# Optimization experiments

Measured on AMD Instinct MI355X. Metric: run time of the kernel, lower is better.

The kernel has to match this reference:

```python
import jax, jax.numpy as jnp
import numpy as np

ALPHA = 0.2  # LeakyReLU negative slope
B, L, FIN, FOUT = 128, 512, 128, 128

def setup_inputs() -> dict:
    key = jax.random.key(0)
    k1, k2, k3, k4, k5 = jax.random.split(key, 5)
    h = jax.random.normal(k1, (B, L, FIN), jnp.float32)
    W = jax.random.normal(k2, (FIN, FOUT), jnp.float32) * (1.0 / np.sqrt(FIN))
    a = jax.random.normal(k3, (2 * FOUT,), jnp.float32) * (1.0 / np.sqrt(2 * FOUT))
    edge_bias = jax.random.normal(k4, (B, L, L), jnp.float32) * 0.1
    adj_mask = jax.random.uniform(k5, (L, L)) > 0.3
    adj_mask = adj_mask | jnp.eye(L, dtype=bool)  # self-loops avoid fully-masked rows
    return {"h": h, "W": W, "a": a, "edge_bias": edge_bias, "adj_mask": adj_mask}

def reference(h, W, a, edge_bias, adj_mask):
    # Wh: [B, L, Fout]
    Wh = jnp.einsum('blf,fo->blo', h, W)
    Fout = W.shape[1]
    # a([Wh_i, Wh_j]) == Wh_i @ a[:Fout] + Wh_j @ a[Fout:]  (avoids O(B*L*L*2F) concat)
    ei = Wh @ a[:Fout]   # [B, L]  (target i contribution)
    ej = Wh @ a[Fout:]   # [B, L]  (source j contribution)
    e = jax.nn.leaky_relu(ei[:, :, None] + ej[:, None, :], ALPHA) + edge_bias  # [B, L, L]
    e = jnp.where(adj_mask[None, :, :], e, -jnp.inf)
    att = jax.nn.softmax(e, axis=-1)  # dropout=0.0 -> identity
    h_prime = jnp.einsum('bij,bjo->bio', att, Wh)  # [B, L, Fout]
    return jax.nn.elu(h_prime)  # concat=True branch
```

## Files before the change

### kernel.cpp

```cpp
#include <hip/hip_runtime.h>
#include <string.h>

#define ALPHA 0.2f

typedef short short8 __attribute__((ext_vector_type(8)));
typedef float floatx4 __attribute__((ext_vector_type(4)));
typedef unsigned short ushort4v __attribute__((ext_vector_type(4)));

__device__ inline unsigned short f2bf(float f) {
    unsigned int v; __builtin_memcpy(&v, &f, 4);
    v = v + 0x7FFFu + ((v >> 16) & 1u);
    return (unsigned short)(v >> 16);
}

#define GLD4(dst, p) asm volatile("global_load_dwordx4 %0, %1, off nt" : "=v"(dst) : "v"(p))

__global__ __launch_bounds__(256, 4) void wh_kernel(const float* __restrict__ h,
                                                    const float* __restrict__ W,
                                                    const float* __restrict__ a,
                                                    const int* __restrict__ adj,
                                                    unsigned short* __restrict__ wht,
                                                    float* __restrict__ ei,
                                                    float* __restrict__ ej,
                                                    unsigned long long* __restrict__ mask)
{
    __shared__ __align__(16) unsigned short w_s[128][136];
    __shared__ float a_s[256];
    const int tid  = threadIdx.x;
    const int lane = tid & 63;
    const int wv   = tid >> 6;
    const int quad = lane >> 4;
    const int l16  = lane & 15;
    const int r0   = blockIdx.x * 128;
    const int b    = r0 >> 9;
    const int jb   = r0 & 511;

    for (int it = 0; it < 64; ++it) {
        int idx = it * 256 + tid;
        w_s[idx & 127][idx >> 7] = f2bf(W[idx]);
    }
    a_s[tid] = a[tid];

    if (blockIdx.x < 128) {
        const int row = blockIdx.x * 4 + wv;
        const int* ar = adj + row * 512;
        unsigned long long wbits[8];
#pragma unroll
        for (int q = 0; q < 8; ++q) wbits[q] = __ballot(ar[q * 64 + lane] != 0);
        if (lane == 0) {
            unsigned long long* mr = mask + row * 8;
#pragma unroll
            for (int q = 0; q < 8; ++q) mr[q] = wbits[q];
        }
    }
    __syncthreads();

    const float* hp0 = h + (size_t)(r0 + wv * 32 + l16) * 128 + quad * 8;
    const float* hp1 = hp0 + 16 * 128;

    floatx4 acc[8][2];
    for (int mo = 0; mo < 8; ++mo)
        for (int n = 0; n < 2; ++n) acc[mo][n] = (floatx4)0.f;

    floatx4 c00 = *(const floatx4*)(hp0);
    floatx4 c01 = *(const floatx4*)(hp0 + 4);
    floatx4 c10 = *(const floatx4*)(hp1);
    floatx4 c11 = *(const floatx4*)(hp1 + 4);
#pragma unroll
    for (int kk = 0; kk < 4; ++kk) {
        floatx4 n00, n01, n10, n11;
        if (kk < 3) {
            n00 = *(const floatx4*)(hp0 + (kk + 1) * 32);
            n01 = *(const floatx4*)(hp0 + (kk + 1) * 32 + 4);
            n10 = *(const floatx4*)(hp1 + (kk + 1) * 32);
            n11 = *(const floatx4*)(hp1 + (kk + 1) * 32 + 4);
        }
        short8 bfr0, bfr1;
#pragma unroll
        for (int e = 0; e < 4; ++e) {
            bfr0[e]     = (short)f2bf(c00[e]);
            bfr0[4 + e] = (short)f2bf(c01[e]);
            bfr1[e]     = (short)f2bf(c10[e]);
            bfr1[4 + e] = (short)f2bf(c11[e]);
        }
#pragma unroll
        for (int mo = 0; mo < 8; ++mo) {
            short8 afr = *(const short8*)&w_s[mo * 16 + l16][kk * 32 + quad * 8];
            acc[mo][0] = __builtin_amdgcn_mfma_f32_16x16x32_bf16(afr, bfr0, acc[mo][0], 0, 0, 0);
            acc[mo][1] = __builtin_amdgcn_mfma_f32_16x16x32_bf16(afr, bfr1, acc[mo][1], 0, 0, 0);
        }
        c00 = n00; c01 = n01; c10 = n10; c11 = n11;
    }

    for (int n = 0; n < 2; ++n) {
        float si = 0.f, sj = 0.f;
        for (int mo = 0; mo < 8; ++mo)
            for (int r = 0; r < 4; ++r) {
                int o = mo * 16 + quad * 4 + r;
                float v = acc[mo][n][r];
                si += v * a_s[o];
                sj += v * a_s[128 + o];
            }
        si += __shfl_xor(si, 16); si += __shfl_xor(si, 32);
        sj += __shfl_xor(sj, 16); sj += __shfl_xor(sj, 32);
        if (quad == 0) {
            int j = jb + wv * 32 + n * 16 + l16;
            ei[b * 512 + j] = si;
            ej[b * 512 + j] = sj;
        }
    }

    for (int mo = 0; mo < 8; ++mo)
        for (int n = 0; n < 2; ++n)
            for (int r = 0; r < 4; ++r) {
                int o = mo * 16 + quad * 4 + r;
                int j = jb + wv * 32 + n * 16 + l16;
                wht[(size_t)b * 65536 + o * 512 + j] = f2bf(acc[mo][n][r]);
            }
}

__global__ __launch_bounds__(512, 4) void attn_kernel(const unsigned short* __restrict__ wht,
                                                      const float* __restrict__ ei,
                                                      const float* __restrict__ ej,
                                                      const float* __restrict__ bias,
                                                      const unsigned* __restrict__ mask32,
                                                      float* __restrict__ out)
{
    __shared__ __align__(16) unsigned short p_s[64][520];
    __shared__ float ei_s[64];
    __shared__ float ej_s[512];
    __shared__ float s_row[64];
    __shared__ unsigned m_s[64][16];

    const int tid  = threadIdx.x;
    const int lane = tid & 63;
    const int wv   = tid >> 6;
    const int quad = lane >> 4;
    const int l16  = lane & 15;

    const int n  = blockIdx.x;
    const int x  = n & 7;
    const int r  = n >> 3;
    const int b  = x * 16 + (r >> 3);
    const int i0 = (r & 7) * 64;

    ej_s[tid] = ej[b * 512 + tid];
    if (tid < 64) ei_s[tid] = ei[b * 512 + i0 + tid];
#pragma unroll
    for (int it = 0; it < 2; ++it) {
        int idx = it * 512 + tid;
        m_s[idx >> 4][idx & 15] = mask32[i0 * 16 + idx];
    }
    __syncthreads();

    const float* bp = bias + ((size_t)(b * 512 + i0 + wv * 8)) * 512;
    const int mw = lane >> 3;
    const int ms = (lane & 7) * 4;

    const floatx4 ejv0 = *(const floatx4*)&ej_s[lane * 4];
    const floatx4 ejv1 = *(const floatx4*)&ej_s[256 + lane * 4];

    floatx4 q0[4], q1[4];
    GLD4(q0[0], bp + lane * 4);            GLD4(q1[0], bp + 256 + lane * 4);
    GLD4(q0[1], bp + 512 + lane * 4);      GLD4(q1[1], bp + 768 + lane * 4);
    GLD4(q0[2], bp + 1024 + lane * 4);     GLD4(q1[2], bp + 1280 + lane * 4);
    GLD4(q0[3], bp + 1536 + lane * 4);     GLD4(q1[3], bp + 1792 + lane * 4);

    float rsum[8];
#pragma unroll
    for (int rr = 0; rr < 8; ++rr) {
        if (rr <= 4)      asm volatile("s_waitcnt vmcnt(6)" ::: "memory");
        else if (rr == 5) asm volatile("s_waitcnt vmcnt(4)" ::: "memory");
        else if (rr == 6) asm volatile("s_waitcnt vmcnt(2)" ::: "memory");
        else              asm volatile("s_waitcnt vmcnt(0)" ::: "memory");
        __builtin_amdgcn_sched_barrier(0);

        const int s  = rr & 3;
        const int il = wv * 8 + rr;
        const float eiv = ei_s[il];
        const unsigned nib0 = (m_s[il][mw]     >> ms) & 0xFu;
        const unsigned nib1 = (m_s[il][8 + mw] >> ms) & 0xFu;
        float sm = 0.f;
        ushort4v p0, p1;
#pragma unroll
        for (int e = 0; e < 4; ++e) {
            float xv = eiv + ejv0[e];
            xv = fmaxf(xv, ALPHA * xv);
            xv += q0[s][e];
            float p = __expf(xv);
            p = (nib0 & (1u << e)) ? p : 0.f;
            sm += p;
            p0[e] = f2bf(p);
        }
#pragma unroll
        for (int e = 0; e < 4; ++e) {
            float xv = eiv + ejv1[e];
            xv = fmaxf(xv, ALPHA * xv);
            xv += q1[s][e];
            float p = __expf(xv);
            p = (nib1 & (1u << e)) ? p : 0.f;
            sm += p;
            p1[e] = f2bf(p);
        }
        *(ushort4v*)&p_s[il][lane * 4]       = p0;
        *(ushort4v*)&p_s[il][256 + lane * 4] = p1;
        rsum[rr] = sm;

        if (rr < 4) {
            GLD4(q0[s], bp + (size_t)(rr + 4) * 512 + lane * 4);
            GLD4(q1[s], bp + (size_t)(rr + 4) * 512 + 256 + lane * 4);
        }
    }

#pragma unroll
    for (int rr = 0; rr < 8; ++rr)
        for (int off = 32; off; off >>= 1)
            rsum[rr] += __shfl_xor(rsum[rr], off);
    if (lane == 0)
#pragma unroll
        for (int rr = 0; rr < 8; ++rr) s_row[wv * 8 + rr] = rsum[rr];
    __syncthreads();

    floatx4 acc[4];
#pragma unroll
    for (int m = 0; m < 4; ++m) acc[m] = (floatx4)0.f;

    const unsigned short* wb = wht + (size_t)b * 65536 + (wv * 16 + l16) * 512 + quad * 8;
    short8 bf = *(const short8*)(wb);
#pragma unroll
    for (int k16 = 0; k16 < 16; ++k16) {
        int ko = k16 * 32 + quad * 8;
        short8 nbf;
        if (k16 < 15) nbf = *(const short8*)(wb + (k16 + 1) * 32);
        short8 af0 = *(const short8*)&p_s[l16][ko];
        short8 af1 = *(const short8*)&p_s[16 + l16][ko];
        short8 af2 = *(const short8*)&p_s[32 + l16][ko];
        short8 af3 = *(const short8*)&p_s[48 + l16][ko];
        acc[0] = __builtin_amdgcn_mfma_f32_16x16x32_bf16(af0, bf, acc[0], 0, 0, 0);
        acc[1] = __builtin_amdgcn_mfma_f32_16x16x32_bf16(af1, bf, acc[1], 0, 0, 0);
        acc[2] = __builtin_amdgcn_mfma_f32_16x16x32_bf16(af2, bf, acc[2], 0, 0, 0);
        acc[3] = __builtin_amdgcn_mfma_f32_16x16x32_bf16(af3, bf, acc[3], 0, 0, 0);
        bf = nbf;
    }

#pragma unroll
    for (int m = 0; m < 4; ++m)
#pragma unroll
        for (int rr2 = 0; rr2 < 4; ++rr2) {
            int il = m * 16 + quad * 4 + rr2;
            int o  = wv * 16 + l16;
            float v = acc[m][rr2] / s_row[il];
            v = v > 0.f ? v : (__expf(v) - 1.f);
            __builtin_nontemporal_store(v, &out[((size_t)(b * 512 + i0 + il)) * 128 + o]);
        }
}

extern "C" void kernel_launch(void* const* d_in, const int* in_sizes, int n_in,
                              void* d_out, int out_size, void* d_ws, size_t ws_size,
                              hipStream_t stream)
{
    const float* h    = (const float*)d_in[0];
    const float* W    = (const float*)d_in[1];
    const float* a    = (const float*)d_in[2];
    const float* bias = (const float*)d_in[3];
    const int*   adj  = (const int*)d_in[4];
    float*       out  = (float*)d_out;

    unsigned short* wht = (unsigned short*)d_ws;
    float* ei = (float*)((char*)d_ws + 16777216);
    float* ej = ei + 65536;
    unsigned long long* mask = (unsigned long long*)((char*)d_ws + 17301504);

    hipLaunchKernelGGL(wh_kernel,   dim3(512),  dim3(256), 0, stream, h, W, a, adj, wht, ei, ej, mask);
    hipLaunchKernelGGL(attn_kernel, dim3(1024), dim3(512), 0, stream, wht, ei, ej, bias,
                       (const unsigned*)mask, out);
}
```

Measured before the change: 241.5 us.

## Warp-specialize attention kernel into producer/consumer waves with double-buffered P tiles

Restructures attn_kernel so each block handles 256 rows of one batch. Four producer waves stream edge_bias and compute masked exp scores into a double-buffered 16-row LDS tile. Four consumer waves run the bf16 MFMA against Wh^T, normalise and apply ELU, and the two groups synchronise with s_barrier per chunk. The aim is to overlap the bandwidth-bound bias streaming with the matmul and to cut the grid to 256 persistent-style blocks. This risks lower occupancy and idle waves if the two phases are unbalanced, and consumers re-read Wh^T from global/L2 on every chunk.

```diff
diff --git a/kernel.cpp b/kernel.cpp
--- a/kernel.cpp
+++ b/kernel.cpp
@@ -119,18 +119,18 @@
             }
 }
 
-__global__ __launch_bounds__(512, 4) void attn_kernel(const unsigned short* __restrict__ wht,
+__global__ __launch_bounds__(512, 2) void attn_kernel(const unsigned short* __restrict__ wht,
                                                       const float* __restrict__ ei,
                                                       const float* __restrict__ ej,
                                                       const float* __restrict__ bias,
                                                       const unsigned* __restrict__ mask32,
                                                       float* __restrict__ out)
 {
-    __shared__ __align__(16) unsigned short p_s[64][520];
-    __shared__ float ei_s[64];
+    __shared__ __align__(16) unsigned short p_s[2][16][520];
+    __shared__ float ei_s[256];
     __shared__ float ej_s[512];
-    __shared__ float s_row[64];
-    __shared__ unsigned m_s[64][16];
+    __shared__ float s_row[2][16];
+    __shared__ unsigned m_s[256][16];
 
     const int tid  = threadIdx.x;
     const int lane = tid & 63;
@@ -138,121 +138,141 @@
     const int quad = lane >> 4;
     const int l16  = lane & 15;
 
-    const int n  = blockIdx.x;
-    const int x  = n & 7;
-    const int r  = n >> 3;
-    const int b  = x * 16 + (r >> 3);
-    const int i0 = (r & 7) * 64;
-
-    ej_s[tid] = ej[b * 512 + tid];
-    if (tid < 64) ei_s[tid] = ei[b * 512 + i0 + tid];
-#pragma unroll
-    for (int it = 0; it < 2; ++it) {
+    const int x     = blockIdx.x & 7;
+    const int r     = blockIdx.x >> 3;
+    const int b     = x * 16 + (r >> 1);
+    const int hrow0 = (r & 1) * 256;
+
+    if (tid < 128) *(floatx4*)&ej_s[tid * 4] = *(const floatx4*)(ej + b * 512 + tid * 4);
+    else if (tid < 384) ei_s[tid - 128] = ei[b * 512 + hrow0 + (tid - 128)];
+#pragma unroll
+    for (int it = 0; it < 8; ++it) {
         int idx = it * 512 + tid;
-        m_s[idx >> 4][idx & 15] = mask32[i0 * 16 + idx];
+        ((unsigned*)m_s)[idx] = mask32[hrow0 * 16 + idx];
     }
     __syncthreads();
 
-    const float* bp = bias + ((size_t)(b * 512 + i0 + wv * 8)) * 512;
     const int mw = lane >> 3;
     const int ms = (lane & 7) * 4;
 
-    const floatx4 ejv0 = *(const floatx4*)&ej_s[lane * 4];
-    const floatx4 ejv1 = *(const floatx4*)&ej_s[256 + lane * 4];
-
-    floatx4 q0[4], q1[4];
-    GLD4(q0[0], bp + lane * 4);            GLD4(q1[0], bp + 256 + lane * 4);
-    GLD4(q0[1], bp + 512 + lane * 4);      GLD4(q1[1], bp + 768 + lane * 4);
-    GLD4(q0[2], bp + 1024 + lane * 4);     GLD4(q1[2], bp + 1280 + lane * 4);
-    GLD4(q0[3], bp + 1536 + lane * 4);     GLD4(q1[3], bp + 1792 + lane * 4);
-
-    float rsum[8];
-#pragma unroll
-    for (int rr = 0; rr < 8; ++rr) {
-        if (rr <= 4)      asm volatile("s_waitcnt vmcnt(6)" ::: "memory");
-        else if (rr == 5) asm volatile("s_waitcnt vmcnt(4)" ::: "memory");
-        else if (rr == 6) asm volatile("s_waitcnt vmcnt(2)" ::: "memory");
-        else              asm volatile("s_waitcnt vmcnt(0)" ::: "memory");
-        __builtin_amdgcn_sched_barrier(0);
-
-        const int s  = rr & 3;
-        const int il = wv * 8 + rr;
-        const float eiv = ei_s[il];
-        const unsigned nib0 = (m_s[il][mw]     >> ms) & 0xFu;
-        const unsigned nib1 = (m_s[il][8 + mw] >> ms) & 0xFu;
-        float sm = 0.f;
-        ushort4v p0, p1;
-#pragma unroll
-        for (int e = 0; e < 4; ++e) {
-            float xv = eiv + ejv0[e];
-            xv = fmaxf(xv, ALPHA * xv);
-            xv += q0[s][e];
-            float p = __expf(xv);
-            p = (nib0 & (1u << e)) ? p : 0.f;
-            sm += p;
-            p0[e] = f2bf(p);
-        }
-#pragma unroll
-        for (int e = 0; e < 4; ++e) {
-            float xv = eiv + ejv1[e];
-            xv = fmaxf(xv, ALPHA * xv);
-            xv += q1[s][e];
-            float p = __expf(xv);
-            p = (nib1 & (1u << e)) ? p : 0.f;
-            sm += p;
-            p1[e] = f2bf(p);
-        }
-        *(ushort4v*)&p_s[il][lane * 4]       = p0;
-        *(ushort4v*)&p_s[il][256 + lane * 4] = p1;
-        rsum[rr] = sm;
-
-        if (rr < 4) {
-            GLD4(q0[s], bp + (size_t)(rr + 4) * 512 + lane * 4);
-            GLD4(q1[s], bp + (size_t)(rr + 4) * 512 + 256 + lane * 4);
-        }
-    }
-
-#pragma unroll
-    for (int rr = 0; rr < 8; ++rr)
-        for (int off = 32; off; off >>= 1)
-            rsum[rr] += __shfl_xor(rsum[rr], off);
-    if (lane == 0)
-#pragma unroll
-        for (int rr = 0; rr < 8; ++rr) s_row[wv * 8 + rr] = rsum[rr];
-    __syncthreads();
-
-    floatx4 acc[4];
-#pragma unroll
-    for (int m = 0; m < 4; ++m) acc[m] = (floatx4)0.f;
-
-    const unsigned short* wb = wht + (size_t)b * 65536 + (wv * 16 + l16) * 512 + quad * 8;
-    short8 bf = *(const short8*)(wb);
-#pragma unroll
-    for (int k16 = 0; k16 < 16; ++k16) {
-        int ko = k16 * 32 + quad * 8;
-        short8 nbf;
-        if (k16 < 15) nbf = *(const short8*)(wb + (k16 + 1) * 32);
-        short8 af0 = *(const short8*)&p_s[l16][ko];
-        short8 af1 = *(const short8*)&p_s[16 + l16][ko];
-        short8 af2 = *(const short8*)&p_s[32 + l16][ko];
-        short8 af3 = *(const short8*)&p_s[48 + l16][ko];
-        acc[0] = __builtin_amdgcn_mfma_f32_16x16x32_bf16(af0, bf, acc[0], 0, 0, 0);
-        acc[1] = __builtin_amdgcn_mfma_f32_16x16x32_bf16(af1, bf, acc[1], 0, 0, 0);
-        acc[2] = __builtin_amdgcn_mfma_f32_16x16x32_bf16(af2, bf, acc[2], 0, 0, 0);
-        acc[3] = __builtin_amdgcn_mfma_f32_16x16x32_bf16(af3, bf, acc[3], 0, 0, 0);
-        bf = nbf;
-    }
-
-#pragma unroll
-    for (int m = 0; m < 4; ++m)
-#pragma unroll
-        for (int rr2 = 0; rr2 < 4; ++rr2) {
-            int il = m * 16 + quad * 4 + rr2;
-            int o  = wv * 16 + l16;
-            float v = acc[m][rr2] / s_row[il];
-            v = v > 0.f ? v : (__expf(v) - 1.f);
-            __builtin_nontemporal_store(v, &out[((size_t)(b * 512 + i0 + il)) * 128 + o]);
-        }
+    if (wv < 4) {
+        const floatx4 ejv0 = *(const floatx4*)&ej_s[lane * 4];
+        const floatx4 ejv1 = *(const floatx4*)&ej_s[256 + lane * 4];
+        const int w = wv;
+        const float* bp = bias + ((size_t)(b * 512 + hrow0 + w * 4)) * 512;
+
+        floatx4 q0[4], q1[4];
+#pragma unroll
+        for (int rr = 0; rr < 4; ++rr) {
+            GLD4(q0[rr], bp + rr * 512 + lane * 4);
+            GLD4(q1[rr], bp + rr * 512 + 256 + lane * 4);
+        }
+
+        for (int c = 0; c < 16; ++c) {
+            const int pb = c & 1;
+            const bool last = (c == 15);
+            float rs[4];
+#pragma unroll
+            for (int rr = 0; rr < 4; ++rr) {
+                if (!last || rr == 0) asm volatile("s_waitcnt vmcnt(6)" ::: "memory");
+                else if (rr == 1)     asm volatile("s_waitcnt vmcnt(4)" ::: "memory");
+                else if (rr == 2)     asm volatile("s_waitcnt vmcnt(2)" ::: "memory");
+                else                  asm volatile("s_waitcnt vmcnt(0)" ::: "memory");
+                __builtin_amdgcn_sched_barrier(0);
+
+                const int il   = w * 4 + rr;
+                const int lrow = c * 16 + il;
+                const float eiv = ei_s[lrow];
+                const unsigned nib0 = (m_s[lrow][mw]     >> ms) & 0xFu;
+                const unsigned nib1 = (m_s[lrow][8 + mw] >> ms) & 0xFu;
+                float sm = 0.f;
+                ushort4v o0, o1;
+#pragma unroll
+                for (int e = 0; e < 4; ++e) {
+                    float xv = eiv + ejv0[e];
+                    xv = fmaxf(xv, ALPHA * xv);
+                    xv += q0[rr][e];
+                    float p = __expf(xv);
+                    p = (nib0 & (1u << e)) ? p : 0.f;
+                    sm += p;
+                    o0[e] = f2bf(p);
+                }
+#pragma unroll
+                for (int e = 0; e < 4; ++e) {
+                    float xv = eiv + ejv1[e];
+                    xv = fmaxf(xv, ALPHA * xv);
+                    xv += q1[rr][e];
+                    float p = __expf(xv);
+                    p = (nib1 & (1u << e)) ? p : 0.f;
+                    sm += p;
+                    o1[e] = f2bf(p);
+                }
+                *(ushort4v*)&p_s[pb][il][lane * 4]       = o0;
+                *(ushort4v*)&p_s[pb][il][256 + lane * 4] = o1;
+                rs[rr] = sm;
+                if (!last) {
+                    GLD4(q0[rr], bp + (16 + rr) * 512 + lane * 4);
+                    GLD4(q1[rr], bp + (16 + rr) * 512 + 256 + lane * 4);
+                }
+            }
+#pragma unroll
+            for (int rr = 0; rr < 4; ++rr) {
+                float v = rs[rr];
+                for (int off = 32; off; off >>= 1) v += __shfl_xor(v, off);
+                if (lane == 0) s_row[pb][w * 4 + rr] = v;
+            }
+            bp += 16 * 512;
+            asm volatile("s_waitcnt lgkmcnt(0)" ::: "memory");
+            __builtin_amdgcn_s_barrier();
+            asm volatile("" ::: "memory");
+        }
+        asm volatile("s_waitcnt lgkmcnt(0)" ::: "memory");
+        __builtin_amdgcn_s_barrier();
+        asm volatile("" ::: "memory");
+    } else {
+        const int w2 = wv - 4;
+        const unsigned short* wb0 = wht + (size_t)b * 65536 + (w2 * 32 + l16) * 512 + quad * 8;
+        const unsigned short* wb1 = wb0 + 16 * 512;
+
+        asm volatile("s_waitcnt lgkmcnt(0)" ::: "memory");
+        __builtin_amdgcn_s_barrier();
+        asm volatile("" ::: "memory");
+
+        for (int c = 0; c < 16; ++c) {
+            const int pb = c & 1;
+            floatx4 acc0 = (floatx4)0.f, acc1 = (floatx4)0.f;
+            short8 bf0 = *(const short8*)(wb0);
+            short8 bf1 = *(const short8*)(wb1);
+#pragma unroll
+            for (int k16 = 0; k16 < 16; ++k16) {
+                int ko = k16 * 32 + quad * 8;
+                short8 nbf0, nbf1;
+                if (k16 < 15) {
+                    nbf0 = *(const short8*)(wb0 + (k16 + 1) * 32);
+                    nbf1 = *(const short8*)(wb1 + (k16 + 1) * 32);
+                }
+                short8 af = *(const short8*)&p_s[pb][l16][ko];
+                acc0 = __builtin_amdgcn_mfma_f32_16x16x32_bf16(af, bf0, acc0, 0, 0, 0);
+                acc1 = __builtin_amdgcn_mfma_f32_16x16x32_bf16(af, bf1, acc1, 0, 0, 0);
+                bf0 = nbf0; bf1 = nbf1;
+            }
+#pragma unroll
+            for (int rr = 0; rr < 4; ++rr) {
+                int il = quad * 4 + rr;
+                float inv = 1.0f / s_row[pb][il];
+                size_t orow = ((size_t)(b * 512 + hrow0 + c * 16 + il)) * 128;
+                float v0 = acc0[rr] * inv;
+                v0 = v0 > 0.f ? v0 : (__expf(v0) - 1.f);
+                __builtin_nontemporal_store(v0, &out[orow + w2 * 32 + l16]);
+                float v1 = acc1[rr] * inv;
+                v1 = v1 > 0.f ? v1 : (__expf(v1) - 1.f);
+                __builtin_nontemporal_store(v1, &out[orow + w2 * 32 + 16 + l16]);
+            }
+            asm volatile("s_waitcnt lgkmcnt(0)" ::: "memory");
+            __builtin_amdgcn_s_barrier();
+            asm volatile("" ::: "memory");
+        }
+    }
 }
 
 extern "C" void kernel_launch(void* const* d_in, const int* in_sizes, int n_in,
@@ -271,7 +291,7 @@
     float* ej = ei + 65536;
     unsigned long long* mask = (unsigned long long*)((char*)d_ws + 17301504);
 
-    hipLaunchKernelGGL(wh_kernel,   dim3(512),  dim3(256), 0, stream, h, W, a, adj, wht, ei, ej, mask);
-    hipLaunchKernelGGL(attn_kernel, dim3(1024), dim3(512), 0, stream, wht, ei, ej, bias,
+    hipLaunchKernelGGL(wh_kernel,   dim3(512), dim3(256), 0, stream, h, W, a, adj, wht, ei, ej, mask);
+    hipLaunchKernelGGL(attn_kernel, dim3(256), dim3(512), 0, stream, wht, ei, ej, bias,
                        (const unsigned*)mask, out);
 }
```

After: 238.5 us. No clear change (-1.2%).
